# Kernel tuning notes

Hardware: AMD Instinct MI355X
Metric: run time of the kernel (lower is better)

## Reference

```python
import jax, jax.numpy as jnp
import numpy as np

NEG_SLOPE = 0.2

def gat_layer(x, src, dst, W, a_src, a_dst, num_nodes):
    """PyG-style GATConv. W:[F_in,H*C], a_src/a_dst:[H,C]. Returns [N,H,C]."""
    H, C = a_src.shape
    h = (x @ W).reshape(num_nodes, H, C)                      # [N,H,C]
    e_src = jnp.sum(h * a_src, axis=-1)                       # [N,H]
    e_dst = jnp.sum(h * a_dst, axis=-1)                       # [N,H]
    e = jax.nn.leaky_relu(e_src[src] + e_dst[dst], NEG_SLOPE) # [E,H]
    # segment softmax over incoming edges of each destination node
    m = jax.ops.segment_max(e, dst, num_segments=num_nodes)
    w = jnp.exp(e - m[dst])
    z = jax.ops.segment_sum(w, dst, num_segments=num_nodes)
    alpha = w / (z[dst] + 1e-16)                               # [E,H]
    msg = h[src] * alpha[:, :, None]                           # [E,H,C]
    return jax.ops.segment_sum(msg, dst, num_segments=num_nodes)


def setup_inputs() -> dict:
    key = jax.random.key(0)
    ks = jax.random.split(key, 16)
    N, E, F_IN, HID, A, G = 50000, 800000, 128, 128, 32, 64
    x = jax.random.normal(ks[0], (N, F_IN), dtype=jnp.float32)
    edge_index = jax.random.randint(ks[1], (2, E), 0, N, dtype=jnp.int32)
    batch = jnp.sort(jax.random.randint(ks[2], (N,), 0, G, dtype=jnp.int32))
    s = 0.1
    W1 = jax.random.normal(ks[3], (F_IN, 2 * HID), jnp.float32) * s
    a_src1 = jax.random.normal(ks[4], (2, HID), jnp.float32) * s
    a_dst1 = jax.random.normal(ks[5], (2, HID), jnp.float32) * s
    b1 = jnp.zeros((2 * HID,), jnp.float32)
    W2 = jax.random.normal(ks[6], (2 * HID, HID), jnp.float32) * s
    a_src2 = jax.random.normal(ks[7], (1, HID), jnp.float32) * s
    a_dst2 = jax.random.normal(ks[8], (1, HID), jnp.float32) * s
    b2 = jnp.zeros((HID,), jnp.float32)
    Wp = jax.random.normal(ks[9], (HID, A), jnp.float32) * s
    bp = jnp.zeros((A,), jnp.float32)
    Wv = jax.random.normal(ks[10], (HID, 1), jnp.float32) * s
    bv = jnp.zeros((1,), jnp.float32)
    return {"x": x, "edge_index": edge_index, "batch": batch,
            "W1": W1, "a_src1": a_src1, "a_dst1": a_dst1, "b1": b1,
            "W2": W2, "a_src2": a_src2, "a_dst2": a_dst2, "b2": b2,
            "Wp": Wp, "bp": bp, "Wv": Wv, "bv": bv}


def reference(x, edge_index, batch, W1, a_src1, a_dst1, b1,
              W2, a_src2, a_dst2, b2, Wp, bp, Wv, bv):
    N = x.shape[0]
    G = 64  # number of graphs in the batch
    # add self-loops (PyG GATConv default)
    loop = jnp.arange(N, dtype=edge_index.dtype)
    src = jnp.concatenate([edge_index[0], loop])
    dst = jnp.concatenate([edge_index[1], loop])
    # layer 1: heads=2, concat=True
    h1 = gat_layer(x, src, dst, W1, a_src1, a_dst1, N)        # [N,2,HID]
    h1 = jax.nn.elu(h1.reshape(N, -1) + b1)                   # [N,2*HID]
    # layer 2: heads=1, concat=False (mean over heads = identity for H=1)
    h2 = gat_layer(h1, src, dst, W2, a_src2, a_dst2, N)       # [N,1,HID]
    h2 = jax.nn.elu(h2.reshape(N, -1) + b2)                   # [N,HID]
    # global mean pool over graphs
    sums = jax.ops.segment_sum(h2, batch, num_segments=G)
    cnt = jax.ops.segment_sum(jnp.ones((N,), h2.dtype), batch, num_segments=G)
    x_pool = sums / jnp.maximum(cnt, 1.0)[:, None]            # [G,HID]
    policy_logits = x_pool @ Wp + bp                          # [G,A]
    state_value = x_pool @ Wv + bv                            # [G,1]
    return (policy_logits, state_value)
```

## Files before the change

### kernel.cpp

```cpp
#include <hip/hip_runtime.h>
#include <hip/hip_bf16.h>
#include <cstdint>


typedef __attribute__((ext_vector_type(8))) short bf16x8;
typedef __attribute__((ext_vector_type(4))) float f32x4;

#define NBLK_H 160
#define BSH 6
#define BMSK 63
#define PCHUNK 256

__device__ __forceinline__ float wave_sum(float v) {
#pragma unroll
    for (int off = 32; off >= 1; off >>= 1) v += __shfl_xor(v, off, 64);
    return v;
}

__device__ __forceinline__ unsigned short f2bf(float f) {
    union { float f; uint32_t u; } c; c.f = f;
    uint32_t u = c.u;
    return (unsigned short)((u + 0x7fffu + ((u >> 16) & 1u)) >> 16);
}

__device__ __forceinline__ float bf2f(unsigned short u) {
    union { uint32_t u; float f; } c; c.u = ((uint32_t)u) << 16;
    return c.f;
}


template <int K, int FOUT>
__device__ __forceinline__ void swizzle_body(const float* __restrict__ W, int ldW, int colOff,
                                             unsigned short* __restrict__ Bsw, int tid) {
    constexpr int CPW = FOUT / 4, NCT = CPW / 16, KST = K / 32;
    if (tid >= K * FOUT / 8) return;
    int lane = tid & 63;
    int rest = tid >> 6;
    int t = rest % KST; rest /= KST;
    int c = rest % NCT; rest /= NCT;
    int cg_ = rest;
    int quad = lane >> 4, lo = lane & 15;
    int col = colOff + cg_ * CPW + c * 16 + lo;
    unsigned short v[8];
#pragma unroll
    for (int j = 0; j < 8; ++j)
        v[j] = f2bf(W[(t * 32 + quad * 8 + j) * ldW + col]);
    ushort4* dst = (ushort4*)(Bsw + (size_t)tid * 8);
    ushort4 o0, o1;
    o0.x = v[0]; o0.y = v[1]; o0.z = v[2]; o0.w = v[3];
    o1.x = v[4]; o1.y = v[5]; o1.z = v[6]; o1.w = v[7];
    dst[0] = o0; dst[1] = o1;
}


__global__ __launch_bounds__(256) void init_kernel(
        const float* __restrict__ W1, const float* __restrict__ W2,
        const float* __restrict__ a_src1, const float* __restrict__ a_dst1,
        unsigned short* __restrict__ B1h0, unsigned short* __restrict__ B1h1,
        unsigned short* __restrict__ B2,
        float* __restrict__ v1s, float* __restrict__ v1d,
        int* __restrict__ zbase, int zn4, int ZB,
        const int* __restrict__ ei, int* __restrict__ hist,
        int E, int ET, int CHUNK, int NB) {
    __shared__ int bins[1024];
    int b = blockIdx.x;
    if (b < 8)        swizzle_body<128, 128>(W1, 256, 0,   B1h0, b * 256 + threadIdx.x);
    else if (b < 16)  swizzle_body<128, 128>(W1, 256, 128, B1h1, (b - 8) * 256 + threadIdx.x);
    else if (b < 32)  swizzle_body<256, 128>(W2, 128, 0,   B2, (b - 16) * 256 + threadIdx.x);
    else if (b == 32) {
        int t = threadIdx.x, h = t >> 7, k = t & 127;
        float vs = 0.f, vd = 0.f;
        for (int c = 0; c < 128; ++c) {
            float w = W1[k * 256 + h * 128 + c];
            vs += w * a_src1[h * 128 + c];
            vd += w * a_dst1[h * 128 + c];
        }
        v1s[h * 128 + k] = vs;
        v1d[h * 128 + k] = vd;
    } else if (b < 33 + ZB) {
        int i = (b - 33) * 256 + threadIdx.x;
        if (i < zn4) ((int4*)zbase)[i] = make_int4(0, 0, 0, 0);
    } else {
        const int blk = b - 33 - ZB;
        for (int t = threadIdx.x; t < NB; t += 256) bins[t] = 0;
        __syncthreads();
        const int start = blk * CHUNK, end = min(ET, start + CHUNK);
        for (int i = start + threadIdx.x; i < end; i += 256) {
            int dst = (i < E) ? ei[E + i] : (i - E);
            atomicAdd(&bins[dst >> BSH], 1);
        }
        __syncthreads();
        for (int t = threadIdx.x; t < NB; t += 256) hist[t * NBLK_H + blk] = bins[t];
    }
}


__global__ __launch_bounds__(256) void scan_attn1(
        int* __restrict__ hist, int* __restrict__ tsum, int M, int TILESH,
        const float* __restrict__ x, const float* __restrict__ v1s,
        const float* __restrict__ v1d, float* __restrict__ es1,
        float* __restrict__ ed1, unsigned short* __restrict__ xbf, int N) {
    __shared__ int buf[256];
    if ((int)blockIdx.x < TILESH) {
        const int t = threadIdx.x;
        const int base = blockIdx.x * 1024 + t * 4;
        int v[4]; int s = 0;
#pragma unroll
        for (int k = 0; k < 4; ++k) { v[k] = (base + k < M) ? hist[base + k] : 0; s += v[k]; }
        buf[t] = s;
        __syncthreads();
#pragma unroll
        for (int off = 1; off < 256; off <<= 1) {
            int xx = (t >= off) ? buf[t - off] : 0;
            __syncthreads();
            buf[t] += xx;
            __syncthreads();
        }
        int run = buf[t] - s;
#pragma unroll
        for (int k = 0; k < 4; ++k) {
            if (base + k < M) hist[base + k] = run;
            run += v[k];
        }
        if (t == 255) tsum[blockIdx.x] = buf[255];
        return;
    }
    int bid = blockIdx.x - TILESH;
    int wid = (bid * 256 + threadIdx.x) >> 6;
    int lane = threadIdx.x & 63;
    if (wid >= N) return;
    float2 xv = *(const float2*)(x + (size_t)wid * 128 + lane * 2);
    float p0s = xv.x * v1s[lane * 2] + xv.y * v1s[lane * 2 + 1];
    float p1s = xv.x * v1s[128 + lane * 2] + xv.y * v1s[128 + lane * 2 + 1];
    float p0d = xv.x * v1d[lane * 2] + xv.y * v1d[lane * 2 + 1];
    float p1d = xv.x * v1d[128 + lane * 2] + xv.y * v1d[128 + lane * 2 + 1];
    p0s = wave_sum(p0s); p1s = wave_sum(p1s);
    p0d = wave_sum(p0d); p1d = wave_sum(p1d);
    if (lane == 0) {
        es1[wid * 2] = p0s; es1[wid * 2 + 1] = p1s;
        ed1[wid * 2] = p0d; ed1[wid * 2 + 1] = p1d;
    }
    ushort2 o; o.x = f2bf(xv.x); o.y = f2bf(xv.y);
    *(ushort2*)(xbf + (size_t)wid * 128 + lane * 2) = o;
}


__global__ __launch_bounds__(256) void part_kernel(const int* __restrict__ ei,
                                                   const int* __restrict__ hist,
                                                   const int* __restrict__ tsum,
                                                   int* __restrict__ bsorted,
                                                   int* __restrict__ segbase,
                                                   int E, int ET, int CHUNK, int NB, int T) {
    __shared__ int sb[256];
    __shared__ int scur[1024];
    const int t = threadIdx.x;
    sb[t] = (t < T) ? tsum[t] : 0;
    __syncthreads();
#pragma unroll
    for (int off = 1; off < 256; off <<= 1) {
        int v = (t >= off) ? sb[t - off] : 0;
        __syncthreads();
        sb[t] += v;
        __syncthreads();
    }
    const int blk = blockIdx.x;
    for (int b = t; b < NB; b += 256) {
        int idx = b * NBLK_H + blk;
        int tile = idx >> 10;
        int v = hist[idx] + (tile ? sb[tile - 1] : 0);
        scur[b] = v;
        if (blk == 0) segbase[b] = v;
    }
    if (blk == 0 && t == 0) segbase[NB] = sb[T - 1];
    __syncthreads();
    const int start = blk * CHUNK, end = min(ET, start + CHUNK);
    for (int i = start + t; i < end; i += 256) {
        int dst = (i < E) ? ei[E + i] : (i - E);
        int src = (i < E) ? ei[i] : dst;
        int pos = atomicAdd(&scur[dst >> BSH], 1);
        bsorted[pos] = (src << BSH) | (dst & BMSK);
    }
}


__global__ __launch_bounds__(256) void bucket_kernel(const int* __restrict__ bsorted,
                                                     const int* __restrict__ segbase,
                                                     int* __restrict__ csr_src,
                                                     int* __restrict__ rowptr,
                                                     int N, int NB) {
    __shared__ int cnt[64];
    __shared__ int excl[64];
    __shared__ int ebuf[2304];
    const int b = blockIdx.x;
    const int gbase = segbase[b];
    const int gend  = segbase[b + 1];
    const int sz = gend - gbase;
    const int t = threadIdx.x;
    if (b == 0 && t == 255) rowptr[N] = segbase[NB];
    if (t < 64) cnt[t] = 0;
    __syncthreads();
    const bool fits = (sz <= 2304);
    if (fits) {
        for (int i = t; i < sz; i += 256) {
            int p = bsorted[gbase + i];
            ebuf[i] = p;
            atomicAdd(&cnt[p & BMSK], 1);
        }
    } else {
        for (int i = t; i < sz; i += 256) {
            int p = bsorted[gbase + i];
            atomicAdd(&cnt[p & BMSK], 1);
        }
    }
    __syncthreads();
    if (t < 64) excl[t] = cnt[t];
    __syncthreads();
    for (int off = 1; off < 64; off <<= 1) {
        int v = (t < 64 && t >= off) ? excl[t - off] : 0;
        __syncthreads();
        if (t < 64) excl[t] += v;
        __syncthreads();
    }
    if (t < 64) {
        int dst = (b << BSH) + t;
        if (dst < N) rowptr[dst] = gbase + excl[t] - cnt[t];
    }
    __syncthreads();
    if (t < 64) cnt[t] = excl[t] - cnt[t];
    __syncthreads();
    if (fits) {
        for (int i = t; i < sz; i += 256) {
            int p = ebuf[i];
            int pos = atomicAdd(&cnt[p & BMSK], 1);
            csr_src[gbase + pos] = p >> BSH;
        }
    } else {
        for (int i = t; i < sz; i += 256) {
            int p = bsorted[gbase + i];
            int pos = atomicAdd(&cnt[p & BMSK], 1);
            csr_src[gbase + pos] = p >> BSH;
        }
    }
}


#define ACC2(U_, WW_, P_, Q_) { float v_;                              \
    v_ = bf2f(U_.x); P_.x += WW_.x * v_; Q_.x += WW_.y * v_;           \
    v_ = bf2f(U_.y); P_.y += WW_.x * v_; Q_.y += WW_.y * v_;           \
    v_ = bf2f(U_.z); P_.z += WW_.x * v_; Q_.z += WW_.y * v_;           \
    v_ = bf2f(U_.w); P_.w += WW_.x * v_; Q_.w += WW_.y * v_; }

__global__ void gat_agg_x(const unsigned short* __restrict__ xbf,
                          const float* __restrict__ es, const float* __restrict__ ed,
                          const int* __restrict__ rowptr, const int* __restrict__ csr_src,
                          unsigned short* __restrict__ aggx, int N, int NPAD) {
    __shared__ int    s_lds[4][2][32];
    __shared__ float2 w_lds[4][2][32];
    const int wave = threadIdx.x >> 6, lane = threadIdx.x & 63;
    const int g = lane >> 5, c = lane & 31;
    const int node = (blockIdx.x * 4 + wave) * 2 + g;
    if (node >= N) return;
    const int rs = rowptr[node], re = rowptr[node + 1];
    const float2 edn = *(const float2*)(ed + node * 2);

    float z0 = 0.f, z1 = 0.f;
    float4 p = {0.f, 0.f, 0.f, 0.f}, q = {0.f, 0.f, 0.f, 0.f};
    for (int i = rs; i < re; i += 32) {
        const int cnt = min(re - i, 32);
        if (c < cnt) {
            int s = csr_src[i + c];
            float2 esv = *(const float2*)(es + s * 2);
            float e0 = esv.x + edn.x; e0 = (e0 > 0.f) ? e0 : 0.2f * e0;
            float e1 = esv.y + edn.y; e1 = (e1 > 0.f) ? e1 : 0.2f * e1;
            float w0 = __expf(e0), w1 = __expf(e1);
            s_lds[wave][g][c] = s;
            w_lds[wave][g][c] = make_float2(w0, w1);
            z0 += w0; z1 += w1;
        }
        int k = 0;
        for (; k + 7 < cnt; k += 8) {
            int s0 = s_lds[wave][g][k + 0], s1 = s_lds[wave][g][k + 1];
            int s2 = s_lds[wave][g][k + 2], s3 = s_lds[wave][g][k + 3];
            int s4 = s_lds[wave][g][k + 4], s5 = s_lds[wave][g][k + 5];
            int s6 = s_lds[wave][g][k + 6], s7 = s_lds[wave][g][k + 7];
            float2 a0 = w_lds[wave][g][k + 0], a1 = w_lds[wave][g][k + 1];
            float2 a2 = w_lds[wave][g][k + 2], a3 = w_lds[wave][g][k + 3];
            float2 a4 = w_lds[wave][g][k + 4], a5 = w_lds[wave][g][k + 5];
            float2 a6 = w_lds[wave][g][k + 6], a7 = w_lds[wave][g][k + 7];
            ushort4 u0 = *(const ushort4*)(xbf + (size_t)s0 * 128 + c * 4);
            ushort4 u1 = *(const ushort4*)(xbf + (size_t)s1 * 128 + c * 4);
            ushort4 u2 = *(const ushort4*)(xbf + (size_t)s2 * 128 + c * 4);
            ushort4 u3 = *(const ushort4*)(xbf + (size_t)s3 * 128 + c * 4);
            ushort4 u4 = *(const ushort4*)(xbf + (size_t)s4 * 128 + c * 4);
            ushort4 u5 = *(const ushort4*)(xbf + (size_t)s5 * 128 + c * 4);
            ushort4 u6 = *(const ushort4*)(xbf + (size_t)s6 * 128 + c * 4);
            ushort4 u7 = *(const ushort4*)(xbf + (size_t)s7 * 128 + c * 4);
            ACC2(u0, a0, p, q);
            ACC2(u1, a1, p, q);
            ACC2(u2, a2, p, q);
            ACC2(u3, a3, p, q);
            ACC2(u4, a4, p, q);
            ACC2(u5, a5, p, q);
            ACC2(u6, a6, p, q);
            ACC2(u7, a7, p, q);
        }
        for (; k < cnt; ++k) {
            int s0 = s_lds[wave][g][k];
            float2 a0 = w_lds[wave][g][k];
            ushort4 u0 = *(const ushort4*)(xbf + (size_t)s0 * 128 + c * 4);
            ACC2(u0, a0, p, q);
        }
    }
#pragma unroll
    for (int off = 16; off >= 1; off >>= 1) {
        z0 += __shfl_xor(z0, off, 64);
        z1 += __shfl_xor(z1, off, 64);
    }
    const float rz0 = 1.f / (z0 + 1e-16f);
    const float rz1 = 1.f / (z1 + 1e-16f);
    ushort4 o;
    o.x = f2bf(p.x * rz0); o.y = f2bf(p.y * rz0);
    o.z = f2bf(p.z * rz0); o.w = f2bf(p.w * rz0);
    *(ushort4*)(aggx + (size_t)node * 128 + c * 4) = o;
    o.x = f2bf(q.x * rz1); o.y = f2bf(q.y * rz1);
    o.z = f2bf(q.z * rz1); o.w = f2bf(q.w * rz1);
    *(ushort4*)(aggx + (size_t)NPAD * 128 + (size_t)node * 128 + c * 4) = o;
}


__global__ __launch_bounds__(256) void gemm12_fused(
        const unsigned short* __restrict__ Abase,
        const unsigned short* __restrict__ B1h0, const unsigned short* __restrict__ B1h1,
        const unsigned short* __restrict__ B2sw,
        const float* __restrict__ b1,
        const float* __restrict__ a_src, const float* __restrict__ a_dst,
        float* __restrict__ es, float* __restrict__ ed,
        unsigned short* __restrict__ C, int N, int NPAD) {
    __shared__ unsigned short h1t[32 * 256];
    __shared__ float lds_ps[4][32];
    __shared__ float lds_pd[4][32];
    const int tid = threadIdx.x;
    const int wave = tid >> 6, lane = tid & 63;
    const int quad = lane >> 4, lo = lane & 15;
    const int n0 = blockIdx.x * 32;
    char* h1b = (char*)h1t;

    {
        const int head = wave >> 1, wh = wave & 1;
        const unsigned short* A = Abase + (size_t)head * NPAD * 128;
        const bf16x8* Bp = (const bf16x8*)(head ? B1h1 : B1h0);
        bf16x8 bf[4][4];
#pragma unroll
        for (int c = 0; c < 4; ++c)
#pragma unroll
            for (int t = 0; t < 4; ++t)
                bf[c][t] = Bp[((wh * 4 + c) * 4 + t) * 64 + lane];
        f32x4 acc[2][4];
#pragma unroll
        for (int r = 0; r < 2; ++r)
#pragma unroll
            for (int c = 0; c < 4; ++c) acc[r][c] = (f32x4){0.f, 0.f, 0.f, 0.f};
#pragma unroll
        for (int r = 0; r < 2; ++r) {
            const unsigned short* Ar = A + (size_t)(n0 + r * 16 + lo) * 128 + quad * 8;
#pragma unroll
            for (int t = 0; t < 4; ++t) {
                bf16x8 af = *(const bf16x8*)(Ar + t * 32);
#pragma unroll
                for (int c = 0; c < 4; ++c)
                    acc[r][c] = __builtin_amdgcn_mfma_f32_16x16x32_bf16(af, bf[c][t],
                                                                       acc[r][c], 0, 0, 0);
            }
        }
#pragma unroll
        for (int r = 0; r < 2; ++r) {
            int rl = r * 16 + quad * 4;
#pragma unroll
            for (int c = 0; c < 4; ++c) {
                int col = head * 128 + wh * 64 + c * 16 + lo;
                float bv = b1[col];
#pragma unroll
                for (int j = 0; j < 4; ++j) {
                    float v = acc[r][c][j] + bv;
                    v = (v > 0.f) ? v : __expf(v) - 1.f;
                    int row = rl + j;
                    *(unsigned short*)(h1b + row * 512 + ((col * 2) ^ ((row & 31) << 4)))
                        = f2bf(v);
                }
            }
        }
    }
    __syncthreads();

    bf16x8 bf2[2][8];
    {
        const bf16x8* Bp2 = (const bf16x8*)B2sw;
#pragma unroll
        for (int c = 0; c < 2; ++c)
#pragma unroll
            for (int t = 0; t < 8; ++t)
                bf2[c][t] = Bp2[((wave * 2 + c) * 8 + t) * 64 + lane];
    }
    f32x4 acc2[2][2];
#pragma unroll
    for (int r = 0; r < 2; ++r)
#pragma unroll
        for (int c = 0; c < 2; ++c) acc2[r][c] = (f32x4){0.f, 0.f, 0.f, 0.f};
#pragma unroll
    for (int r = 0; r < 2; ++r) {
        const int row = r * 16 + lo;
        const int rsw = (row & 31) << 4;
#pragma unroll
        for (int t = 0; t < 8; ++t) {
            bf16x8 af = *(const bf16x8*)(h1b + row * 512 + (((quad * 8 + t * 32) * 2) ^ rsw));
#pragma unroll
            for (int c = 0; c < 2; ++c)
                acc2[r][c] = __builtin_amdgcn_mfma_f32_16x16x32_bf16(af, bf2[c][t],
                                                                    acc2[r][c], 0, 0, 0);
        }
    }
    const int c0 = wave * 32;
#pragma unroll
    for (int r = 0; r < 2; ++r) {
        int row = n0 + r * 16 + quad * 4;
#pragma unroll
        for (int c = 0; c < 2; ++c) {
            int col = c0 + c * 16 + lo;
#pragma unroll
            for (int j = 0; j < 4; ++j)
                if (row + j < N) C[(size_t)(row + j) * 128 + col] = f2bf(acc2[r][c][j]);
        }
    }
    float asv[2], adv[2];
#pragma unroll
    for (int c = 0; c < 2; ++c) {
        int col = c0 + c * 16 + lo;
        asv[c] = a_src[col];
        adv[c] = a_dst[col];
    }
#pragma unroll
    for (int r = 0; r < 2; ++r) {
#pragma unroll
        for (int j = 0; j < 4; ++j) {
            float ps = 0.f, pd = 0.f;
#pragma unroll
            for (int c = 0; c < 2; ++c) { ps += acc2[r][c][j] * asv[c]; pd += acc2[r][c][j] * adv[c]; }
#pragma unroll
            for (int off = 1; off <= 8; off <<= 1) {
                ps += __shfl_xor(ps, off, 64);
                pd += __shfl_xor(pd, off, 64);
            }
            if (lo == 0) {
                int row_l = r * 16 + quad * 4 + j;
                lds_ps[wave][row_l] = ps;
                lds_pd[wave][row_l] = pd;
            }
        }
    }
    __syncthreads();
    if (tid < 32) {
        int row = tid;
        int n = n0 + row;
        if (n < N) {
            es[n] = lds_ps[0][row] + lds_ps[1][row] + lds_ps[2][row] + lds_ps[3][row];
            ed[n] = lds_pd[0][row] + lds_pd[1][row] + lds_pd[2][row] + lds_pd[3][row];
        }
    }
}


#define ACC1(U_, W_, P_) {                                   \
    P_.x += W_ * bf2f(U_.x); P_.y += W_ * bf2f(U_.y);        \
    P_.z += W_ * bf2f(U_.z); P_.w += W_ * bf2f(U_.w); }

__global__ void gat_agg_h1(const unsigned short* __restrict__ Hpre,
                           const float* __restrict__ es, const float* __restrict__ ed,
                           const int* __restrict__ rowptr, const int* __restrict__ csr_src,
                           const float* __restrict__ bias, unsigned short* __restrict__ out,
                           int N) {
    __shared__ int   s_lds[4][2][32];
    __shared__ float w_lds[4][2][32];
    const int wave = threadIdx.x >> 6, lane = threadIdx.x & 63;
    const int g = lane >> 5, c = lane & 31;
    const int node = (blockIdx.x * 4 + wave) * 2 + g;
    if (node >= N) return;
    const int rs = rowptr[node], re = rowptr[node + 1];
    const float edn = ed[node];

    float z = 0.f;
    float4 p = {0.f, 0.f, 0.f, 0.f};
    for (int i = rs; i < re; i += 32) {
        const int cnt = min(re - i, 32);
        if (c < cnt) {
            int s = csr_src[i + c];
            float e = es[s] + edn;
            e = (e > 0.f) ? e : 0.2f * e;
            float ww = __expf(e);
            s_lds[wave][g][c] = s;
            w_lds[wave][g][c] = ww;
            z += ww;
        }
        int k = 0;
        for (; k + 7 < cnt; k += 8) {
            int s0 = s_lds[wave][g][k + 0], s1 = s_lds[wave][g][k + 1];
            int s2 = s_lds[wave][g][k + 2], s3 = s_lds[wave][g][k + 3];
            int s4 = s_lds[wave][g][k + 4], s5 = s_lds[wave][g][k + 5];
            int s6 = s_lds[wave][g][k + 6], s7 = s_lds[wave][g][k + 7];
            float a0 = w_lds[wave][g][k + 0], a1 = w_lds[wave][g][k + 1];
            float a2 = w_lds[wave][g][k + 2], a3 = w_lds[wave][g][k + 3];
            float a4 = w_lds[wave][g][k + 4], a5 = w_lds[wave][g][k + 5];
            float a6 = w_lds[wave][g][k + 6], a7 = w_lds[wave][g][k + 7];
            ushort4 u0 = *(const ushort4*)(Hpre + (size_t)s0 * 128 + c * 4);
            ushort4 u1 = *(const ushort4*)(Hpre + (size_t)s1 * 128 + c * 4);
            ushort4 u2 = *(const ushort4*)(Hpre + (size_t)s2 * 128 + c * 4);
            ushort4 u3 = *(const ushort4*)(Hpre + (size_t)s3 * 128 + c * 4);
            ushort4 u4 = *(const ushort4*)(Hpre + (size_t)s4 * 128 + c * 4);
            ushort4 u5 = *(const ushort4*)(Hpre + (size_t)s5 * 128 + c * 4);
            ushort4 u6 = *(const ushort4*)(Hpre + (size_t)s6 * 128 + c * 4);
            ushort4 u7 = *(const ushort4*)(Hpre + (size_t)s7 * 128 + c * 4);
            ACC1(u0, a0, p);
            ACC1(u1, a1, p);
            ACC1(u2, a2, p);
            ACC1(u3, a3, p);
            ACC1(u4, a4, p);
            ACC1(u5, a5, p);
            ACC1(u6, a6, p);
            ACC1(u7, a7, p);
        }
        for (; k < cnt; ++k) {
            int s0 = s_lds[wave][g][k];
            float a0 = w_lds[wave][g][k];
            ushort4 u0 = *(const ushort4*)(Hpre + (size_t)s0 * 128 + c * 4);
            ACC1(u0, a0, p);
        }
    }
#pragma unroll
    for (int off = 16; off >= 1; off >>= 1) z += __shfl_xor(z, off, 64);
    const float rz = 1.f / (z + 1e-16f);
    float4 bv = ((const float4*)bias)[c];
    float ox = p.x * rz + bv.x, oy = p.y * rz + bv.y;
    float oz = p.z * rz + bv.z, ow = p.w * rz + bv.w;
    ox = (ox > 0.f) ? ox : __expf(ox) - 1.f;
    oy = (oy > 0.f) ? oy : __expf(oy) - 1.f;
    oz = (oz > 0.f) ? oz : __expf(oz) - 1.f;
    ow = (ow > 0.f) ? ow : __expf(ow) - 1.f;
    ushort4 o;
    o.x = f2bf(ox); o.y = f2bf(oy); o.z = f2bf(oz); o.w = f2bf(ow);
    *(ushort4*)(out + (size_t)node * 128 + c * 4) = o;
}


__global__ __launch_bounds__(256) void pool_partial(const unsigned short* __restrict__ h2,
                                                    const int* __restrict__ batch,
                                                    float* __restrict__ xsum,
                                                    int* __restrict__ cnt, int N) {
    const int base = blockIdx.x * PCHUNK;
    const int rg = threadIdx.x >> 6;
    const int c2 = threadIdx.x & 63;
    float ax = 0.f, ay = 0.f;
    int gcur = -1, run = 0;
    for (int r = rg; r < PCHUNK; r += 4) {
        int i = base + r;
        if (i >= N) break;
        int g = batch[i];
        if (g != gcur) {
            if (gcur >= 0) {
                atomicAdd(&xsum[gcur * 128 + c2 * 2 + 0], ax);
                atomicAdd(&xsum[gcur * 128 + c2 * 2 + 1], ay);
                if (c2 == 0) atomicAdd(&cnt[gcur], run);
            }
            gcur = g; ax = 0.f; ay = 0.f; run = 0;
        }
        ushort2 u = *(const ushort2*)(h2 + (size_t)i * 128 + c2 * 2);
        ax += bf2f(u.x); ay += bf2f(u.y);
        run += 1;
    }
    if (gcur >= 0) {
        atomicAdd(&xsum[gcur * 128 + c2 * 2 + 0], ax);
        atomicAdd(&xsum[gcur * 128 + c2 * 2 + 1], ay);
        if (c2 == 0) atomicAdd(&cnt[gcur], run);
    }
}


__global__ void head_kernel(const float* __restrict__ xsum, const int* __restrict__ cnt,
                            const float* __restrict__ Wp, const float* __restrict__ bp,
                            const float* __restrict__ Wv, const float* __restrict__ bv,
                            float* __restrict__ out) {
    int g = blockIdx.x, t = threadIdx.x;
    __shared__ float p[128];
    float inv = 1.f / fmaxf((float)cnt[g], 1.f);
    p[t] = xsum[g * 128 + t] * inv;
    p[t + 64] = xsum[g * 128 + t + 64] * inv;
    __syncthreads();
    if (t < 32) {
        float acc = bp[t];
        for (int k = 0; k < 128; ++k) acc += p[k] * Wp[k * 32 + t];
        out[g * 32 + t] = acc;
    } else if (t == 32) {
        float acc = bv[0];
        for (int k = 0; k < 128; ++k) acc += p[k] * Wv[k];
        out[64 * 32 + g] = acc;
    }
}


extern "C" void kernel_launch(void* const* d_in, const int* in_sizes, int n_in,
                              void* d_out, int out_size, void* d_ws, size_t ws_size,
                              hipStream_t stream) {
    const float* x      = (const float*)d_in[0];
    const int*   ei     = (const int*)d_in[1];
    const int*   batch  = (const int*)d_in[2];
    const float* W1     = (const float*)d_in[3];
    const float* a_src1 = (const float*)d_in[4];
    const float* a_dst1 = (const float*)d_in[5];
    const float* b1     = (const float*)d_in[6];
    const float* W2     = (const float*)d_in[7];
    const float* a_src2 = (const float*)d_in[8];
    const float* a_dst2 = (const float*)d_in[9];
    const float* b2     = (const float*)d_in[10];
    const float* Wp     = (const float*)d_in[11];
    const float* bp     = (const float*)d_in[12];
    const float* Wv     = (const float*)d_in[13];
    const float* bv     = (const float*)d_in[14];

    const int N  = in_sizes[0] / 128;
    const int E  = in_sizes[1] / 2;
    const int ET = E + N;
    const int NPAD = ((N + 63) / 64) * 64;
    const int NBLK32 = NPAD / 32;
    const int PBLK = (N + PCHUNK - 1) / PCHUNK;
    const int NB = (N + 63) >> BSH;
    const int CHUNK = (ET + NBLK_H - 1) / NBLK_H;
    const int M = NB * NBLK_H;
    const int TILESH = (M + 1023) / 1024;
    const int AB = (N + 3) / 4;
    const int GB = (N + 7) / 8;

    char* ws = (char*)d_ws;
    size_t off = 0;
    auto alloc = [&](size_t bytes) -> void* {
        void* p = ws + off;
        off = (off + bytes + 255) & ~(size_t)255;
        return p;
    };
    unsigned short* xbf   = (unsigned short*)alloc((size_t)NPAD * 128 * 2);
    unsigned short* aggx  = (unsigned short*)alloc((size_t)2 * NPAD * 128 * 2);
    unsigned short* h2pre = (unsigned short*)alloc((size_t)NPAD * 128 * 2);
    unsigned short* h2bf  = (unsigned short*)alloc((size_t)N * 128 * 2);
    unsigned short* w1h0  = (unsigned short*)alloc((size_t)128 * 128 * 2);
    unsigned short* w1h1  = (unsigned short*)alloc((size_t)128 * 128 * 2);
    unsigned short* w2sw  = (unsigned short*)alloc((size_t)256 * 128 * 2);
    float* v1s = (float*)alloc(256 * 4);
    float* v1d = (float*)alloc(256 * 4);
    float* es1 = (float*)alloc((size_t)N * 2 * 4);
    float* ed1 = (float*)alloc((size_t)N * 2 * 4);
    float* es2 = (float*)alloc((size_t)N * 4);
    float* ed2 = (float*)alloc((size_t)N * 4);
    const int ZINTS = 64 * 128 + 64;
    int*   zbase  = (int*)alloc(((size_t)ZINTS + 8) * 4);
    float* xsum   = (float*)zbase;
    int*   cnt    = (int*)(xsum + 64 * 128);
    int*    rowptr    = (int*)alloc((size_t)(N + 1) * 4);
    int*    hist      = (int*)alloc((size_t)M * 4);
    int*    segbase   = (int*)alloc((size_t)(NB + 1) * 4);
    int*    bsorted   = (int*)alloc((size_t)ET * 4);
    int*    csrsrc    = (int*)alloc((size_t)ET * 4);
    int*    tsum      = (int*)alloc(256 * 4);
    const int zn4 = (ZINTS + 3) / 4;
    const int ZB = (zn4 + 255) / 256;

    init_kernel<<<33 + ZB + NBLK_H, 256, 0, stream>>>(W1, W2, a_src1, a_dst1,
                                                      w1h0, w1h1, w2sw, v1s, v1d,
                                                      zbase, zn4, ZB,
                                                      ei, hist, E, ET, CHUNK, NB);
    scan_attn1<<<TILESH + AB, 256, 0, stream>>>(hist, tsum, M, TILESH,
                                                x, v1s, v1d, es1, ed1, xbf, N);
    part_kernel<<<NBLK_H, 256, 0, stream>>>(ei, hist, tsum, bsorted, segbase,
                                            E, ET, CHUNK, NB, TILESH);
    bucket_kernel<<<NB, 256, 0, stream>>>(bsorted, segbase, csrsrc, rowptr, N, NB);
    gat_agg_x<<<GB, 256, 0, stream>>>(xbf, es1, ed1, rowptr, csrsrc, aggx, N, NPAD);
    gemm12_fused<<<NBLK32, 256, 0, stream>>>(aggx, w1h0, w1h1, w2sw, b1,
                                             a_src2, a_dst2, es2, ed2, h2pre, N, NPAD);
    gat_agg_h1<<<GB, 256, 0, stream>>>(h2pre, es2, ed2, rowptr, csrsrc, b2, h2bf, N);
    pool_partial<<<PBLK, 256, 0, stream>>>(h2bf, batch, xsum, cnt, N);
    head_kernel<<<64, 64, 0, stream>>>(xsum, cnt, Wp, bp, Wv, bv, (float*)d_out);
}
```

Baseline: 273.0 us.

## Fuse CSR bucket build with layer-1 aggregation and halve bucket width

The bucket-sort kernel that builds the per-node CSR is merged with the first-layer attention aggregation kernel. Each block now handles 32 destination nodes instead of 64, builds their CSR segment, and then aggregates those nodes directly, with row starts kept in shared memory. This removes one kernel launch and the rowptr round-trip between the two kernels. The cost is less parallelism in the aggregation phase (4 iterations of 8 nodes per block), and the histogram and shared-memory arrays double in size to cover the larger bucket count.

```diff
diff --git a/kernel.cpp b/kernel.cpp
--- a/kernel.cpp
+++ b/kernel.cpp
@@ -7,8 +7,8 @@
 typedef __attribute__((ext_vector_type(4))) float f32x4;
 
 #define NBLK_H 160
-#define BSH 6
-#define BMSK 63
+#define BSH 5
+#define BMSK 31
 #define PCHUNK 256
 
 __device__ __forceinline__ float wave_sum(float v) {
@@ -62,7 +62,7 @@
         int* __restrict__ zbase, int zn4, int ZB,
         const int* __restrict__ ei, int* __restrict__ hist,
         int E, int ET, int CHUNK, int NB) {
-    __shared__ int bins[1024];
+    __shared__ int bins[2048];
     int b = blockIdx.x;
     if (b < 8)        swizzle_body<128, 128>(W1, 256, 0,   B1h0, b * 256 + threadIdx.x);
     else if (b < 16)  swizzle_body<128, 128>(W1, 256, 128, B1h1, (b - 8) * 256 + threadIdx.x);
@@ -152,7 +152,7 @@
                                                    int* __restrict__ segbase,
                                                    int E, int ET, int CHUNK, int NB, int T) {
     __shared__ int sb[256];
-    __shared__ int scur[1024];
+    __shared__ int scur[2048];
     const int t = threadIdx.x;
     sb[t] = (t < T) ? tsum[t] : 0;
     __syncthreads();
@@ -183,50 +183,54 @@
 }
 
 
-__global__ __launch_bounds__(256) void bucket_kernel(const int* __restrict__ bsorted,
-                                                     const int* __restrict__ segbase,
-                                                     int* __restrict__ csr_src,
-                                                     int* __restrict__ rowptr,
-                                                     int N, int NB) {
-    __shared__ int cnt[64];
-    __shared__ int excl[64];
-    __shared__ int ebuf[2304];
+#define ACC2(U_, WW_, P_, Q_) { float v_;                              \
+    v_ = bf2f(U_.x); P_.x += WW_.x * v_; Q_.x += WW_.y * v_;           \
+    v_ = bf2f(U_.y); P_.y += WW_.x * v_; Q_.y += WW_.y * v_;           \
+    v_ = bf2f(U_.z); P_.z += WW_.x * v_; Q_.z += WW_.y * v_;           \
+    v_ = bf2f(U_.w); P_.w += WW_.x * v_; Q_.w += WW_.y * v_; }
+
+__global__ __launch_bounds__(256) void bucket_agg(
+        const int* __restrict__ bsorted, const int* __restrict__ segbase,
+        const unsigned short* __restrict__ xbf,
+        const float* __restrict__ es, const float* __restrict__ ed,
+        int* __restrict__ csr_src, int* __restrict__ rowptr,
+        unsigned short* __restrict__ aggx, int N, int NB, int NPAD) {
+    __shared__ int cnt[32], excl[32];
+    __shared__ int rstart[33];
+    __shared__ int ebuf[1152];
+    __shared__ int    s_lds[4][2][32];
+    __shared__ float2 w_lds[4][2][32];
     const int b = blockIdx.x;
-    const int gbase = segbase[b];
-    const int gend  = segbase[b + 1];
+    const int gbase = segbase[b], gend = segbase[b + 1];
     const int sz = gend - gbase;
     const int t = threadIdx.x;
     if (b == 0 && t == 255) rowptr[N] = segbase[NB];
-    if (t < 64) cnt[t] = 0;
-    __syncthreads();
-    const bool fits = (sz <= 2304);
-    if (fits) {
-        for (int i = t; i < sz; i += 256) {
-            int p = bsorted[gbase + i];
-            ebuf[i] = p;
-            atomicAdd(&cnt[p & BMSK], 1);
-        }
-    } else {
-        for (int i = t; i < sz; i += 256) {
-            int p = bsorted[gbase + i];
-            atomicAdd(&cnt[p & BMSK], 1);
-        }
-    }
-    __syncthreads();
-    if (t < 64) excl[t] = cnt[t];
-    __syncthreads();
-    for (int off = 1; off < 64; off <<= 1) {
-        int v = (t < 64 && t >= off) ? excl[t - off] : 0;
+    if (t < 32) cnt[t] = 0;
+    __syncthreads();
+    const bool fits = (sz <= 1152);
+    for (int i = t; i < sz; i += 256) {
+        int p = bsorted[gbase + i];
+        if (fits) ebuf[i] = p;
+        atomicAdd(&cnt[p & BMSK], 1);
+    }
+    __syncthreads();
+    if (t < 32) excl[t] = cnt[t];
+    __syncthreads();
+    for (int off = 1; off < 32; off <<= 1) {
+        int v = (t < 32 && t >= off) ? excl[t - off] : 0;
         __syncthreads();
-        if (t < 64) excl[t] += v;
+        if (t < 32) excl[t] += v;
         __syncthreads();
     }
-    if (t < 64) {
+    if (t < 32) {
+        int rst = gbase + excl[t] - cnt[t];
+        rstart[t] = rst;
         int dst = (b << BSH) + t;
-        if (dst < N) rowptr[dst] = gbase + excl[t] - cnt[t];
-    }
-    __syncthreads();
-    if (t < 64) cnt[t] = excl[t] - cnt[t];
+        if (dst < N) rowptr[dst] = rst;
+        cnt[t] = excl[t] - cnt[t];
+    } else if (t == 32) {
+        rstart[32] = gend;
+    }
     __syncthreads();
     if (fits) {
         for (int i = t; i < sz; i += 256) {
@@ -241,90 +245,80 @@
             csr_src[gbase + pos] = p >> BSH;
         }
     }
-}
-
-
-#define ACC2(U_, WW_, P_, Q_) { float v_;                              \
-    v_ = bf2f(U_.x); P_.x += WW_.x * v_; Q_.x += WW_.y * v_;           \
-    v_ = bf2f(U_.y); P_.y += WW_.x * v_; Q_.y += WW_.y * v_;           \
-    v_ = bf2f(U_.z); P_.z += WW_.x * v_; Q_.z += WW_.y * v_;           \
-    v_ = bf2f(U_.w); P_.w += WW_.x * v_; Q_.w += WW_.y * v_; }
-
-__global__ void gat_agg_x(const unsigned short* __restrict__ xbf,
-                          const float* __restrict__ es, const float* __restrict__ ed,
-                          const int* __restrict__ rowptr, const int* __restrict__ csr_src,
-                          unsigned short* __restrict__ aggx, int N, int NPAD) {
-    __shared__ int    s_lds[4][2][32];
-    __shared__ float2 w_lds[4][2][32];
-    const int wave = threadIdx.x >> 6, lane = threadIdx.x & 63;
+    __syncthreads();
+
+    const int wave = t >> 6, lane = t & 63;
     const int g = lane >> 5, c = lane & 31;
-    const int node = (blockIdx.x * 4 + wave) * 2 + g;
-    if (node >= N) return;
-    const int rs = rowptr[node], re = rowptr[node + 1];
-    const float2 edn = *(const float2*)(ed + node * 2);
-
-    float z0 = 0.f, z1 = 0.f;
-    float4 p = {0.f, 0.f, 0.f, 0.f}, q = {0.f, 0.f, 0.f, 0.f};
-    for (int i = rs; i < re; i += 32) {
-        const int cnt = min(re - i, 32);
-        if (c < cnt) {
-            int s = csr_src[i + c];
-            float2 esv = *(const float2*)(es + s * 2);
-            float e0 = esv.x + edn.x; e0 = (e0 > 0.f) ? e0 : 0.2f * e0;
-            float e1 = esv.y + edn.y; e1 = (e1 > 0.f) ? e1 : 0.2f * e1;
-            float w0 = __expf(e0), w1 = __expf(e1);
-            s_lds[wave][g][c] = s;
-            w_lds[wave][g][c] = make_float2(w0, w1);
-            z0 += w0; z1 += w1;
-        }
-        int k = 0;
-        for (; k + 7 < cnt; k += 8) {
-            int s0 = s_lds[wave][g][k + 0], s1 = s_lds[wave][g][k + 1];
-            int s2 = s_lds[wave][g][k + 2], s3 = s_lds[wave][g][k + 3];
-            int s4 = s_lds[wave][g][k + 4], s5 = s_lds[wave][g][k + 5];
-            int s6 = s_lds[wave][g][k + 6], s7 = s_lds[wave][g][k + 7];
-            float2 a0 = w_lds[wave][g][k + 0], a1 = w_lds[wave][g][k + 1];
-            float2 a2 = w_lds[wave][g][k + 2], a3 = w_lds[wave][g][k + 3];
-            float2 a4 = w_lds[wave][g][k + 4], a5 = w_lds[wave][g][k + 5];
-            float2 a6 = w_lds[wave][g][k + 6], a7 = w_lds[wave][g][k + 7];
-            ushort4 u0 = *(const ushort4*)(xbf + (size_t)s0 * 128 + c * 4);
-            ushort4 u1 = *(const ushort4*)(xbf + (size_t)s1 * 128 + c * 4);
-            ushort4 u2 = *(const ushort4*)(xbf + (size_t)s2 * 128 + c * 4);
-            ushort4 u3 = *(const ushort4*)(xbf + (size_t)s3 * 128 + c * 4);
-            ushort4 u4 = *(const ushort4*)(xbf + (size_t)s4 * 128 + c * 4);
-            ushort4 u5 = *(const ushort4*)(xbf + (size_t)s5 * 128 + c * 4);
-            ushort4 u6 = *(const ushort4*)(xbf + (size_t)s6 * 128 + c * 4);
-            ushort4 u7 = *(const ushort4*)(xbf + (size_t)s7 * 128 + c * 4);
-            ACC2(u0, a0, p, q);
-            ACC2(u1, a1, p, q);
-            ACC2(u2, a2, p, q);
-            ACC2(u3, a3, p, q);
-            ACC2(u4, a4, p, q);
-            ACC2(u5, a5, p, q);
-            ACC2(u6, a6, p, q);
-            ACC2(u7, a7, p, q);
-        }
-        for (; k < cnt; ++k) {
-            int s0 = s_lds[wave][g][k];
-            float2 a0 = w_lds[wave][g][k];
-            ushort4 u0 = *(const ushort4*)(xbf + (size_t)s0 * 128 + c * 4);
-            ACC2(u0, a0, p, q);
-        }
-    }
-#pragma unroll
-    for (int off = 16; off >= 1; off >>= 1) {
-        z0 += __shfl_xor(z0, off, 64);
-        z1 += __shfl_xor(z1, off, 64);
-    }
-    const float rz0 = 1.f / (z0 + 1e-16f);
-    const float rz1 = 1.f / (z1 + 1e-16f);
-    ushort4 o;
-    o.x = f2bf(p.x * rz0); o.y = f2bf(p.y * rz0);
-    o.z = f2bf(p.z * rz0); o.w = f2bf(p.w * rz0);
-    *(ushort4*)(aggx + (size_t)node * 128 + c * 4) = o;
-    o.x = f2bf(q.x * rz1); o.y = f2bf(q.y * rz1);
-    o.z = f2bf(q.z * rz1); o.w = f2bf(q.w * rz1);
-    *(ushort4*)(aggx + (size_t)NPAD * 128 + (size_t)node * 128 + c * 4) = o;
+#pragma unroll 1
+    for (int it = 0; it < 4; ++it) {
+        const int local = it * 8 + wave * 2 + g;
+        const int node = (b << BSH) + local;
+        if (node >= N) continue;
+        const int rs = rstart[local], re = rstart[local + 1];
+        const float2 edn = *(const float2*)(ed + node * 2);
+        float z0 = 0.f, z1 = 0.f;
+        float4 p = {0.f, 0.f, 0.f, 0.f}, q = {0.f, 0.f, 0.f, 0.f};
+        for (int i = rs; i < re; i += 32) {
+            const int cc = min(re - i, 32);
+            if (c < cc) {
+                int s = csr_src[i + c];
+                float2 esv = *(const float2*)(es + s * 2);
+                float e0 = esv.x + edn.x; e0 = (e0 > 0.f) ? e0 : 0.2f * e0;
+                float e1 = esv.y + edn.y; e1 = (e1 > 0.f) ? e1 : 0.2f * e1;
+                float w0 = __expf(e0), w1 = __expf(e1);
+                s_lds[wave][g][c] = s;
+                w_lds[wave][g][c] = make_float2(w0, w1);
+                z0 += w0; z1 += w1;
+            }
+            int k = 0;
+            for (; k + 7 < cc; k += 8) {
+                int s0 = s_lds[wave][g][k + 0], s1 = s_lds[wave][g][k + 1];
+                int s2 = s_lds[wave][g][k + 2], s3 = s_lds[wave][g][k + 3];
+                int s4 = s_lds[wave][g][k + 4], s5 = s_lds[wave][g][k + 5];
+                int s6 = s_lds[wave][g][k + 6], s7 = s_lds[wave][g][k + 7];
+                float2 a0 = w_lds[wave][g][k + 0], a1 = w_lds[wave][g][k + 1];
+                float2 a2 = w_lds[wave][g][k + 2], a3 = w_lds[wave][g][k + 3];
+                float2 a4 = w_lds[wave][g][k + 4], a5 = w_lds[wave][g][k + 5];
+                float2 a6 = w_lds[wave][g][k + 6], a7 = w_lds[wave][g][k + 7];
+                ushort4 u0 = *(const ushort4*)(xbf + (size_t)s0 * 128 + c * 4);
+                ushort4 u1 = *(const ushort4*)(xbf + (size_t)s1 * 128 + c * 4);
+                ushort4 u2 = *(const ushort4*)(xbf + (size_t)s2 * 128 + c * 4);
+                ushort4 u3 = *(const ushort4*)(xbf + (size_t)s3 * 128 + c * 4);
+                ushort4 u4 = *(const ushort4*)(xbf + (size_t)s4 * 128 + c * 4);
+                ushort4 u5 = *(const ushort4*)(xbf + (size_t)s5 * 128 + c * 4);
+                ushort4 u6 = *(const ushort4*)(xbf + (size_t)s6 * 128 + c * 4);
+                ushort4 u7 = *(const ushort4*)(xbf + (size_t)s7 * 128 + c * 4);
+                ACC2(u0, a0, p, q);
+                ACC2(u1, a1, p, q);
+                ACC2(u2, a2, p, q);
+                ACC2(u3, a3, p, q);
+                ACC2(u4, a4, p, q);
+                ACC2(u5, a5, p, q);
+                ACC2(u6, a6, p, q);
+                ACC2(u7, a7, p, q);
+            }
+            for (; k < cc; ++k) {
+                int s0 = s_lds[wave][g][k];
+                float2 a0 = w_lds[wave][g][k];
+                ushort4 u0 = *(const ushort4*)(xbf + (size_t)s0 * 128 + c * 4);
+                ACC2(u0, a0, p, q);
+            }
+        }
+#pragma unroll
+        for (int off = 16; off >= 1; off >>= 1) {
+            z0 += __shfl_xor(z0, off, 64);
+            z1 += __shfl_xor(z1, off, 64);
+        }
+        const float rz0 = 1.f / (z0 + 1e-16f);
+        const float rz1 = 1.f / (z1 + 1e-16f);
+        ushort4 o;
+        o.x = f2bf(p.x * rz0); o.y = f2bf(p.y * rz0);
+        o.z = f2bf(p.z * rz0); o.w = f2bf(p.w * rz0);
+        *(ushort4*)(aggx + (size_t)node * 128 + c * 4) = o;
+        o.x = f2bf(q.x * rz1); o.y = f2bf(q.y * rz1);
+        o.z = f2bf(q.z * rz1); o.w = f2bf(q.w * rz1);
+        *(ushort4*)(aggx + (size_t)NPAD * 128 + (size_t)node * 128 + c * 4) = o;
+    }
 }
 
 
@@ -630,7 +624,7 @@
     const int NPAD = ((N + 63) / 64) * 64;
     const int NBLK32 = NPAD / 32;
     const int PBLK = (N + PCHUNK - 1) / PCHUNK;
-    const int NB = (N + 63) >> BSH;
+    const int NB = (N + BMSK) >> BSH;
     const int CHUNK = (ET + NBLK_H - 1) / NBLK_H;
     const int M = NB * NBLK_H;
     const int TILESH = (M + 1023) / 1024;
@@ -678,8 +672,8 @@
                                                 x, v1s, v1d, es1, ed1, xbf, N);
     part_kernel<<<NBLK_H, 256, 0, stream>>>(ei, hist, tsum, bsorted, segbase,
                                             E, ET, CHUNK, NB, TILESH);
-    bucket_kernel<<<NB, 256, 0, stream>>>(bsorted, segbase, csrsrc, rowptr, N, NB);
-    gat_agg_x<<<GB, 256, 0, stream>>>(xbf, es1, ed1, rowptr, csrsrc, aggx, N, NPAD);
+    bucket_agg<<<NB, 256, 0, stream>>>(bsorted, segbase, xbf, es1, ed1,
+                                       csrsrc, rowptr, aggx, N, NB, NPAD);
     gemm12_fused<<<NBLK32, 256, 0, stream>>>(aggx, w1h0, w1h1, w2sw, b1,
                                              a_src2, a_dst2, es2, ed2, h2pre, N, NPAD);
     gat_agg_h1<<<GB, 256, 0, stream>>>(h2pre, es2, ed2, rowptr, csrsrc, b2, h2bf, N);
```

Measured after the change: 279.0 us. 1.02x slower.
